# Kernel optimization log

Hardware: AMD Instinct MI355X
Metric: run time of the kernel (lower is better)

Reference implementation:

```python
import jax, jax.numpy as jnp
from jax import lax
import numpy as np

B, N, E, U = 128, 1024, 300, 128
L = 512          # num_leaves per sample
NN = 2 * L - 1   # num_nodes per sample (binary tree)


def _hsig(x):
    # Keras hard_sigmoid: clip(0.2*x + 0.5, 0, 1)
    return jnp.clip(0.2 * x + 0.5, 0.0, 1.0)


def setup_inputs() -> dict:
    key = jax.random.key(0)
    ks = jax.random.split(key, 5)
    rng = np.random.default_rng(0)
    # children of node t are uniform in [0, t) -> valid bottom-up binary tree
    u = rng.random((B, N, 2))
    child = (u * np.arange(N)[None, :, None]).astype(np.int32)
    child[:, :L, :] = 0  # leaves have no children (never read)
    num_vecs = np.tile(np.array([[NN, L]], np.int32), (B, 1))
    return {
        "initial_state": jax.random.normal(ks[0], (B, N, E), jnp.float32),
        "translation_kernel": jax.random.normal(ks[1], (E, U), jnp.float32) * 0.05,
        "kernel": jax.random.normal(ks[2], (5 * U, U), jnp.float32) * 0.05,
        "recurrent_kernel": jax.random.normal(ks[3], (5 * U, 2 * U), jnp.float32) * 0.05,
        "bias": jnp.zeros((5 * U, 1), jnp.float32),
        "child_vecs": jnp.asarray(child),
        "num_vecs": jnp.asarray(num_vecs),
    }


def reference(initial_state, translation_kernel, kernel, recurrent_kernel, bias,
              child_vecs, num_vecs):
    b, n, _ = initial_state.shape
    units = kernel.shape[1]
    # leaf initial states: relu(x @ W_translate)  -> [B, N, U]
    x = jax.nn.relu(jnp.einsum('bne,eu->bnu', initial_state, translation_kernel))
    num_nodes = num_vecs[:, 0]
    num_leaves = num_vecs[:, 1]
    bvec = bias[:, 0][None, :]  # [1, 5U]

    def step(carry, t):
        H, C = carry  # [B, N, U] each
        ch = jnp.take(child_vecs, t, axis=1)                                   # [B, 2]
        h_ch = jnp.take_along_axis(H, ch[:, :, None], axis=1).reshape(b, 2 * units)
        c_ch = jnp.take_along_axis(C, ch[:, :, None], axis=1).reshape(b, 2 * units)
        xt = jnp.take(x, t, axis=1)                                            # [B, U]
        # z = kernel @ x^T + recurrent_kernel @ [h_l; h_r] + bias  (batched, [B, 5U])
        z = xt @ kernel.T + h_ch @ recurrent_kernel.T + bvec
        i = _hsig(z[:, :units])
        f = _hsig(z[:, units:3 * units])                                       # [B, 2U]
        o = _hsig(z[:, 3 * units:4 * units])
        g = jnp.tanh(z[:, 4 * units:])
        # faithful to original: reshape (flat_mem*f) as [U, 2] row-major, sum axis 1
        c_new = (c_ch * f).reshape(b, units, 2).sum(axis=-1) + i * g
        h_new = o * jnp.tanh(c_new)
        act = ((t >= num_leaves) & (t < num_nodes))[:, None]                   # [B, 1]
        h_upd = jnp.where(act, h_new, jnp.take(H, t, axis=1))
        c_upd = jnp.where(act, c_new, jnp.take(C, t, axis=1))
        H = lax.dynamic_update_slice(H, h_upd[:, None, :], (0, t, 0))
        C = lax.dynamic_update_slice(C, c_upd[:, None, :], (0, t, 0))
        return (H, C), None

    # leaves start with hidden = memory = translated vec; internal nodes overwritten in order
    (H, _), _ = lax.scan(step, (x, x), jnp.arange(n))
    valid = (jnp.arange(n)[None, :] < num_nodes[:, None])[..., None]
    return H * valid.astype(H.dtype)
```

## Files before the change

### kernel.cpp

```cpp
#include <hip/hip_runtime.h>
#include <hip/hip_bf16.h>

#define B_ 128
#define N_ 1024
#define E_ 300
#define U_ 128
#define M_ (B_ * N_)
#define Z_ (5 * U_)
#define LMAXT 40
#define LPAR 20

typedef __attribute__((ext_vector_type(8))) short bf16x8;
typedef __attribute__((ext_vector_type(4))) float f32x4;
typedef _Float16 f16x4 __attribute__((ext_vector_type(4)));
typedef _Float16 f16x8 __attribute__((ext_vector_type(8)));

__device__ __forceinline__ short f2bf(float f) {
  unsigned u = __builtin_bit_cast(unsigned, f);
  u = (u + 0x7fffu + ((u >> 16) & 1u)) >> 16;
  return (short)u;
}

__device__ __forceinline__ float hsig(float z) {
  float v = __builtin_fmaf(z, 0.2f, 0.5f);
  v = v < 0.f ? 0.f : v;
  v = v > 1.f ? 1.f : v;
  return v;
}

__device__ __forceinline__ float tanh_fast(float x) {
  float p = __expf(2.f * x);
  return 1.f - 2.f * __builtin_amdgcn_rcpf(p + 1.f);
}

__device__ __forceinline__ unsigned pk2(float a, float b) {
  return __builtin_bit_cast(unsigned, __builtin_amdgcn_cvt_pkrtz(a, b));
}

__device__ __forceinline__ f16x8 pack8(float4 a, float4 b) {
  uint4 u;
  u.x = pk2(a.x, a.y);
  u.y = pk2(a.z, a.w);
  u.z = pk2(b.x, b.y);
  u.w = pk2(b.z, b.w);
  return __builtin_bit_cast(f16x8, u);
}

__global__ __launch_bounds__(256) void prep(
    const float* __restrict__ Wr, const float* __restrict__ Wk,
    _Float16* __restrict__ W16, _Float16* __restrict__ Wk16) {
  const int idx = blockIdx.x * 256 + threadIdx.x;
  if (idx < 163840) {
    W16[idx] = (_Float16)Wr[idx];
  } else if (idx < 245760) {
    const int i = idx - 163840;
    Wk16[i] = (_Float16)Wk[i];
  }
}

__global__ __launch_bounds__(256) void x_gemm(
    const float* __restrict__ A, const float* __restrict__ W,
    float* __restrict__ H) {
  __shared__ __align__(16) short As[64][40];
  __shared__ __align__(16) short Ws[128][40];
  const int tid = threadIdx.x;
  const int m0 = blockIdx.x * 64;
  f32x4 acc[8] = {};
  const int lane = tid & 63, wv = tid >> 6;
  const int lr = lane & 15, lg = lane >> 4;

  for (int kc = 0; kc < 10; ++kc) {
    const int k0 = kc * 32;
    {
      const int row = tid >> 2, kk = (tid & 3) * 8;
      const float* src = A + (size_t)(m0 + row) * E_ + k0 + kk;
      bf16x8 v;
      if (k0 + 32 <= E_) {
#pragma unroll
        for (int i = 0; i < 8; ++i) v[i] = f2bf(src[i]);
      } else {
#pragma unroll
        for (int i = 0; i < 8; ++i)
          v[i] = (k0 + kk + i < E_) ? f2bf(src[i]) : (short)0;
      }
      *(bf16x8*)&As[row][kk] = v;
    }
#pragma unroll
    for (int s = 0; s < 2; ++s) {
      const int slot = tid + s * 256;
      const int n = slot & 127, kg = slot >> 7;
      bf16x8 v;
      if (k0 + 32 <= E_) {
#pragma unroll
        for (int i = 0; i < 8; ++i) v[i] = f2bf(W[(k0 + kg * 8 + i) * U_ + n]);
      } else {
#pragma unroll
        for (int i = 0; i < 8; ++i) {
          const int k = k0 + kg * 8 + i;
          v[i] = (k < E_) ? f2bf(W[k * U_ + n]) : (short)0;
        }
      }
      *(bf16x8*)&Ws[n][kg * 8] = v;
    }
    __syncthreads();
    bf16x8 a = *(const bf16x8*)&As[wv * 16 + lr][lg * 8];
#pragma unroll
    for (int nt = 0; nt < 8; ++nt) {
      bf16x8 b = *(const bf16x8*)&Ws[nt * 16 + lr][lg * 8];
      acc[nt] = __builtin_amdgcn_mfma_f32_16x16x32_bf16(a, b, acc[nt], 0, 0, 0);
    }
    __syncthreads();
  }
#pragma unroll
  for (int nt = 0; nt < 8; ++nt) {
#pragma unroll
    for (int r = 0; r < 4; ++r) {
      const int m = m0 + wv * 16 + lg * 4 + r;
      const int n = nt * 16 + lr;
      float v = acc[nt][r];
      v = v > 0.f ? v : 0.f;
      H[(size_t)m * U_ + n] = v;
    }
  }
}

__global__ __launch_bounds__(256) void xz_gemm(
    const float* __restrict__ X, const _Float16* __restrict__ Wk16,
    const float* __restrict__ bias, const int* __restrict__ nv,
    _Float16* __restrict__ XZ) {
  const int m0 = blockIdx.x * 64;
  {
    const int bb = m0 >> 10;
    const int t0 = m0 & (N_ - 1);
    const int nodes = nv[2 * bb], leaves = nv[2 * bb + 1];
    if (t0 + 64 <= leaves || t0 >= nodes) return;
  }
  __shared__ __align__(16) short As[64][40];
  __shared__ __align__(16) short Ws[128][40];
  __shared__ __align__(16) _Float16 xzls[64][136];
  const int tid = threadIdx.x;
  const int n0 = blockIdx.y * 128;
  f32x4 acc[8] = {};
  const int lane = tid & 63, wv = tid >> 6;
  const int lr = lane & 15, lg = lane >> 4;

  for (int kc = 0; kc < 4; ++kc) {
    const int k0 = kc * 32;
    {
      const int row = tid >> 2, kk = (tid & 3) * 8;
      const float* src = X + (size_t)(m0 + row) * U_ + k0 + kk;
      const float4 a0 = *(const float4*)src;
      const float4 a1 = *(const float4*)(src + 4);
      *(f16x8*)&As[row][kk] = pack8(a0, a1);
    }
#pragma unroll
    for (int s = 0; s < 2; ++s) {
      const int slot = tid + s * 256;
      const int n = slot >> 2, kk = (slot & 3) * 8;
      *(f16x8*)&Ws[n][kk] =
          *(const f16x8*)(Wk16 + (size_t)(n0 + n) * U_ + k0 + kk);
    }
    __syncthreads();
    f16x8 a = *(const f16x8*)&As[wv * 16 + lr][lg * 8];
#pragma unroll
    for (int nt = 0; nt < 8; ++nt) {
      f16x8 b = *(const f16x8*)&Ws[nt * 16 + lr][lg * 8];
      acc[nt] = __builtin_amdgcn_mfma_f32_16x16x32_f16(a, b, acc[nt], 0, 0, 0);
    }
    __syncthreads();
  }
#pragma unroll
  for (int nt = 0; nt < 8; ++nt) {
    const float bv = bias[n0 + nt * 16 + lr];
#pragma unroll
    for (int r = 0; r < 4; ++r)
      xzls[wv * 16 + lg * 4 + r][nt * 16 + lr] = (_Float16)(acc[nt][r] + bv);
  }
  __syncthreads();
  {
    const int row = tid >> 2, c0 = (tid & 3) * 32;
    _Float16* dst = XZ + (size_t)(m0 + row) * Z_ + n0 + c0;
#pragma unroll
    for (int s = 0; s < 4; ++s)
      *(f16x8*)(dst + 8 * s) = *(const f16x8*)&xzls[row][c0 + 8 * s];
  }
}

__global__ __launch_bounds__(512) void levelize(
    const int* __restrict__ child, const int* __restrict__ nv,
    unsigned char* __restrict__ lv, short* __restrict__ rank,
    int* __restrict__ cnt) {
  const int b = blockIdx.x;
  const int tid = threadIdx.x;
  int nodes = nv[2 * b];
  int leaves = nv[2 * b + 1];
  if (nodes > N_) nodes = N_;
  if (leaves < 0) leaves = 0;

  __shared__ short lvs[N_];
  __shared__ int chs[2 * N_];
  __shared__ int cnts[LMAXT];
  __shared__ int changed;

  for (int i = tid; i < N_; i += 512) lvs[i] = 0;
  for (int i = tid; i < 2 * N_; i += 512) chs[i] = child[(size_t)b * 2 * N_ + i];
  if (tid < LMAXT) cnts[tid] = 0;
  __syncthreads();

  int stable = 0;
  for (int s = 0; s < 64; ++s) {
    if (tid == 0) changed = 0;
    __syncthreads();
    int any = 0;
    for (int t = leaves + tid; t < nodes; t += 512) {
      const int c0 = chs[2 * t], c1 = chs[2 * t + 1];
      const int l0 = (c0 < t && c0 >= 0) ? lvs[c0] : 0;
      const int l1 = (c1 < t && c1 >= 0) ? lvs[c1] : 0;
      const int l = 1 + (l0 > l1 ? l0 : l1);
      if (l > (int)lvs[t]) { lvs[t] = (short)l; any = 1; }
    }
    if (any) changed = 1;
    __syncthreads();
    if (!changed) { stable = 1; break; }
  }
  if (!stable) {
    if (tid == 0) {
      for (int t = leaves; t < nodes; ++t) {
        const int c0 = chs[2 * t], c1 = chs[2 * t + 1];
        const int l0 = (c0 < t && c0 >= 0) ? lvs[c0] : 0;
        const int l1 = (c1 < t && c1 >= 0) ? lvs[c1] : 0;
        lvs[t] = (short)(1 + (l0 > l1 ? l0 : l1));
      }
    }
    __syncthreads();
  }

  for (int t = tid; t < nodes; t += 512) {
    int l = (t < leaves) ? 0 : (int)lvs[t];
    if (l > LMAXT - 1) l = LMAXT - 1;
    lv[b * N_ + t] = (unsigned char)l;
    if (t >= leaves && l < LMAXT - 1)
      rank[b * N_ + t] = (short)atomicAdd(&cnts[l], 1);
  }
  __syncthreads();
  if (tid == 0) {
    for (int t = leaves; t < nodes; ++t)
      if ((int)lvs[t] >= LMAXT - 1) rank[b * N_ + t] = (short)(cnts[LMAXT - 1]++);
  }
  __syncthreads();
  if (tid < LMAXT) cnt[tid * 128 + b] = cnts[tid];
}

__global__ __launch_bounds__(64) void offsets(
    const int* __restrict__ cnt, int* __restrict__ pos, int* __restrict__ goff) {
  const int l = threadIdx.x;
  __shared__ int tot[LMAXT];
  if (l < LMAXT) {
    int s = 0;
    for (int b = 0; b < 128; ++b) {
      pos[l * 128 + b] = s;
      s += cnt[l * 128 + b];
    }
    tot[l] = s;
  }
  __syncthreads();
  if (l == 0) {
    int g = 0;
    for (int i = 0; i < LMAXT; ++i) { goff[i] = g; g += tot[i]; }
    goff[LMAXT] = g;
  }
  __syncthreads();
  if (l < LMAXT) {
    const int g = goff[l];
    for (int b = 0; b < 128; ++b) pos[l * 128 + b] += g;
  }
}

__global__ __launch_bounds__(256) void scatter_zero(
    const int* __restrict__ nv, const unsigned char* __restrict__ lv,
    const short* __restrict__ rank, const int* __restrict__ pos,
    int* __restrict__ glist, float* __restrict__ H) {
  const int b = blockIdx.x;
  const int tid = threadIdx.x;
  int nodes = nv[2 * b];
  int leaves = nv[2 * b + 1];
  if (nodes > N_) nodes = N_;
  if (leaves < 0) leaves = 0;
  for (int t = leaves + tid; t < nodes; t += 256) {
    const int l = lv[b * N_ + t];
    glist[pos[l * 128 + b] + rank[b * N_ + t]] = (b << 10) | t;
  }
  const int total = (N_ - nodes) * U_;
  for (int idx = tid; idx < total; idx += 256)
    H[(size_t)b * N_ * U_ + nodes * U_ + idx] = 0.f;
}

struct ChunkLd {
  float4 a0, a1;
  float4 cv0, cv1;
  f16x4 xzi, xzo, xzg;
  f16x8 xzf;
  int nid, rem;
};

__device__ __forceinline__ ChunkLd load_chunk(
    int chunk, int nchunk, int base, int count, const int* __restrict__ glist,
    const int* __restrict__ child, const unsigned char* __restrict__ lv,
    const _Float16* __restrict__ XZ, const float* __restrict__ H,
    const float* __restrict__ C, int j, int s, int col, int u0, int mc) {
  ChunkLd r;
  const int cc = chunk < nchunk - 1 ? chunk : nchunk - 1;
  const int cb = base + cc * 16;
  int rem = count - cc * 16;
  if (rem > 16) rem = 16;
  r.rem = rem;

  const int nidj = glist[cb + (j < rem ? j : rem - 1)];
  const int bj = nidj >> 10, tj = nidj & 1023;
  const int chj = child[((size_t)bj << 11) + 2 * tj + (s >> 4)];
  const float* hsrc = H + (((size_t)(bj << 10) + chj) << 7) + ((s & 15) << 3);
  r.a0 = *(const float4*)hsrc;
  r.a1 = *(const float4*)(hsrc + 4);

  const int nidc = glist[cb + (col < rem ? col : rem - 1)];
  r.nid = nidc;
  const _Float16* xzr = XZ + (size_t)nidc * Z_;
  r.xzi = *(const f16x4*)(xzr + u0);
  r.xzf = *(const f16x8*)(xzr + 128 + mc);
  r.xzo = *(const f16x4*)(xzr + 384 + u0);
  r.xzg = *(const f16x4*)(xzr + 512 + u0);
  const int bc = nidc >> 10, tc = nidc & 1023;
  const int csel = child[((size_t)bc << 11) + 2 * tc + (mc >> 7)];
  const int crow = (bc << 10) | csel;
  const float* cbp =
      (lv[crow] == 0 ? H : C) + ((size_t)crow << 7) + (mc & 127);
  r.cv0 = ((const float4*)cbp)[0];
  r.cv1 = ((const float4*)cbp)[1];
  return r;
}

__global__ __launch_bounds__(512, 2) void level_gemm(
    int lvl, const _Float16* __restrict__ W16, const int* __restrict__ child,
    const unsigned char* __restrict__ lv, const int* __restrict__ goff,
    const int* __restrict__ glist, const _Float16* __restrict__ XZ,
    float* __restrict__ H, float* __restrict__ C) {
  const int base = goff[lvl];
  const int count = goff[lvl + 1] - base;
  if (count <= 0) return;
  const int nchunk = (count + 15) >> 4;
  if ((int)blockIdx.x >= nchunk) return;
  const int tid = threadIdx.x;
  const int lane = tid & 63, w = tid >> 6;
  const int col = lane & 15, hi = lane >> 4;
  const int u0 = 16 * w + 4 * hi;
  const int mc = 2 * u0;
  const int j = tid >> 5, s = tid & 31;

  f16x8 afrag[5][8];
  {
    const int rows[5] = {16 * w + col, 128 + 32 * w + 2 * col,
                         129 + 32 * w + 2 * col, 384 + 16 * w + col,
                         512 + 16 * w + col};
#pragma unroll
    for (int rt = 0; rt < 5; ++rt) {
      const _Float16* rs = W16 + (size_t)rows[rt] * 256 + 8 * hi;
#pragma unroll
      for (int kt = 0; kt < 8; ++kt) afrag[rt][kt] = *(const f16x8*)(rs + 32 * kt);
    }
  }

  __shared__ __align__(16) _Float16 hbuf[2][16][272];

  ChunkLd cur = load_chunk(blockIdx.x, nchunk, base, count, glist, child, lv,
                           XZ, H, C, j, s, col, u0, mc);
  int p = 0;
  for (int chunk = blockIdx.x; chunk < nchunk; chunk += gridDim.x) {
    uint4 hp;
    hp.x = pk2(cur.a0.x, cur.a0.y);
    hp.y = pk2(cur.a0.z, cur.a0.w);
    hp.z = pk2(cur.a1.x, cur.a1.y);
    hp.w = pk2(cur.a1.z, cur.a1.w);
    *(uint4*)&hbuf[p][j][(s >> 4) * 128 + (s & 15) * 8] = hp;

    ChunkLd nxt = load_chunk(chunk + gridDim.x < nchunk ? chunk + gridDim.x
                                                        : nchunk - 1,
                             nchunk, base, count, glist, child, lv, XZ, H, C,
                             j, s, col, u0, mc);

    asm volatile("s_waitcnt lgkmcnt(0)" ::: "memory");
    __builtin_amdgcn_sched_barrier(0);
    __builtin_amdgcn_s_barrier();
    __builtin_amdgcn_sched_barrier(0);

    f32x4 acc[5];
#pragma unroll
    for (int r = 0; r < 4; ++r) {
      acc[0][r] = (float)cur.xzi[r];
      acc[1][r] = (float)cur.xzf[2 * r];
      acc[2][r] = (float)cur.xzf[2 * r + 1];
      acc[3][r] = (float)cur.xzo[r];
      acc[4][r] = (float)cur.xzg[r];
    }
#pragma unroll
    for (int kt = 0; kt < 8; ++kt) {
      const f16x8 bf = *(const f16x8*)&hbuf[p][col][32 * kt + 8 * hi];
#pragma unroll
      for (int rt = 0; rt < 5; ++rt)
        acc[rt] = __builtin_amdgcn_mfma_f32_16x16x32_f16(afrag[rt][kt], bf,
                                                         acc[rt], 0, 0, 0);
    }

    const float ce[8] = {cur.cv0.x, cur.cv0.y, cur.cv0.z, cur.cv0.w,
                         cur.cv1.x, cur.cv1.y, cur.cv1.z, cur.cv1.w};
    f32x4 hn4, cn4;
#pragma unroll
    for (int r = 0; r < 4; ++r) {
      const float cn = ce[2 * r] * hsig(acc[1][r]) +
                       ce[2 * r + 1] * hsig(acc[2][r]) +
                       hsig(acc[0][r]) * tanh_fast(acc[4][r]);
      cn4[r] = cn;
      hn4[r] = hsig(acc[3][r]) * tanh_fast(cn);
    }
    if (col < cur.rem) {
      const size_t rowb = (size_t)cur.nid << 7;
      *(f32x4*)(H + rowb + u0) = hn4;
      *(f32x4*)(C + rowb + u0) = cn4;
    }
    cur = nxt;
    p ^= 1;
  }
}

__global__ __launch_bounds__(512, 2) void tail_scan(
    const _Float16* __restrict__ W16, const int* __restrict__ child,
    const unsigned char* __restrict__ lv, const int* __restrict__ nv,
    const int* __restrict__ pos, const int* __restrict__ cnt,
    const int* __restrict__ glist, const _Float16* __restrict__ XZ,
    float* __restrict__ H, float* __restrict__ C) {
  const int b = blockIdx.x;
  const int tid = threadIdx.x;
  const int lane = tid & 63, w = tid >> 6;
  const int col = lane & 15, hi = lane >> 4;
  const int u0 = 16 * w + 4 * hi;
  const int mc = 2 * u0;
  const int m4 = 4 * lane;

  f16x8 afrag[5][8];
  {
    const int rows[5] = {16 * w + col, 128 + 32 * w + 2 * col,
                         129 + 32 * w + 2 * col, 384 + 16 * w + col,
                         512 + 16 * w + col};
#pragma unroll
    for (int rt = 0; rt < 5; ++rt) {
      const _Float16* rs = W16 + (size_t)rows[rt] * 256 + 8 * hi;
#pragma unroll
      for (int kt = 0; kt < 8; ++kt) afrag[rt][kt] = *(const f16x8*)(rs + 32 * kt);
    }
  }

  __shared__ __align__(16) _Float16 hb1[256];
  const int* chb = child + (size_t)b * 2 * N_;
  const unsigned char* lvb = lv + (size_t)b * N_;
  float* Hb = H + (size_t)b * N_ * U_;
  float* Cb = C + (size_t)b * N_ * U_;
  const _Float16* xzb = XZ + (size_t)b * N_ * Z_;

  for (int l = LPAR; l < LMAXT; ++l) {
    const int p0 = pos[l * 128 + b];
    const int n = cnt[l * 128 + b];
    for (int i = 0; i < n; ++i) {
      const int t = glist[p0 + i] & 1023;
      if (tid < 64) {
        const int ch = chb[2 * t + (m4 >> 7)];
        const float4 hv = *(const float4*)(Hb + ((size_t)ch << 7) + (m4 & 127));
        uint2 hp;
        hp.x = pk2(hv.x, hv.y);
        hp.y = pk2(hv.z, hv.w);
        *(uint2*)&hb1[m4] = hp;
      }
      const int cs = chb[2 * t + (mc >> 7)];
      const float* cbp =
          (lvb[cs] == 0 ? Hb : Cb) + ((size_t)cs << 7) + (mc & 127);
      const float4 cv0 = ((const float4*)cbp)[0];
      const float4 cv1 = ((const float4*)cbp)[1];
      const _Float16* xzr = xzb + (size_t)t * Z_;
      const f16x4 xzi = *(const f16x4*)(xzr + u0);
      const f16x8 xzf = *(const f16x8*)(xzr + 128 + mc);
      const f16x4 xzo = *(const f16x4*)(xzr + 384 + u0);
      const f16x4 xzg = *(const f16x4*)(xzr + 512 + u0);
      __syncthreads();
      f32x4 acc[5];
#pragma unroll
      for (int r = 0; r < 4; ++r) {
        acc[0][r] = (float)xzi[r];
        acc[1][r] = (float)xzf[2 * r];
        acc[2][r] = (float)xzf[2 * r + 1];
        acc[3][r] = (float)xzo[r];
        acc[4][r] = (float)xzg[r];
      }
#pragma unroll
      for (int kt = 0; kt < 8; ++kt) {
        const f16x8 bf = *(const f16x8*)&hb1[32 * kt + 8 * hi];
#pragma unroll
        for (int rt = 0; rt < 5; ++rt)
          acc[rt] = __builtin_amdgcn_mfma_f32_16x16x32_f16(afrag[rt][kt], bf,
                                                           acc[rt], 0, 0, 0);
      }
      const float ce[8] = {cv0.x, cv0.y, cv0.z, cv0.w,
                           cv1.x, cv1.y, cv1.z, cv1.w};
      f32x4 hn4, cn4;
#pragma unroll
      for (int r = 0; r < 4; ++r) {
        const float cn = ce[2 * r] * hsig(acc[1][r]) +
                         ce[2 * r + 1] * hsig(acc[2][r]) +
                         hsig(acc[0][r]) * tanh_fast(acc[4][r]);
        cn4[r] = cn;
        hn4[r] = hsig(acc[3][r]) * tanh_fast(cn);
      }
      if (col == 0) {
        *(f32x4*)(Hb + ((size_t)t << 7) + u0) = hn4;
        *(f32x4*)(Cb + ((size_t)t << 7) + u0) = cn4;
      }
      __syncthreads();
    }
  }
}

extern "C" void kernel_launch(void* const* d_in, const int* in_sizes, int n_in,
                              void* d_out, int out_size, void* d_ws,
                              size_t ws_size, hipStream_t stream) {
  const float* state = (const float*)d_in[0];
  const float* tk    = (const float*)d_in[1];
  const float* Wk    = (const float*)d_in[2];
  const float* Wr    = (const float*)d_in[3];
  const float* bias  = (const float*)d_in[4];
  const int*   child = (const int*)d_in[5];
  const int*   nvp   = (const int*)d_in[6];
  float* H = (float*)d_out;

  char* wsb = (char*)d_ws;
  _Float16* W16   = (_Float16*)(wsb + 0x000000);
  _Float16* Wk16  = (_Float16*)(wsb + 0x050000);
  unsigned char* lv = (unsigned char*)(wsb + 0x078000);
  short* rank     = (short*)(wsb + 0x098000);
  int* cnt        = (int*)(wsb + 0x0D8000);
  int* pos        = (int*)(wsb + 0x0DD000);
  int* goff       = (int*)(wsb + 0x0E2000);
  int* glist      = (int*)(wsb + 0x0E3000);
  const size_t meta_sz = 2ull * 1024 * 1024;
  const size_t c_bytes = (size_t)M_ * U_ * sizeof(float);
  float* C = (float*)(wsb + meta_sz);
  _Float16* XZ = (_Float16*)(wsb + meta_sz + c_bytes);

  prep<<<960, 256, 0, stream>>>(Wr, Wk, W16, Wk16);
  x_gemm<<<M_ / 64, 256, 0, stream>>>(state, tk, H);
  xz_gemm<<<dim3(M_ / 64, 5), 256, 0, stream>>>(H, Wk16, bias, nvp, XZ);
  levelize<<<B_, 512, 0, stream>>>(child, nvp, lv, rank, cnt);
  offsets<<<1, 64, 0, stream>>>(cnt, pos, goff);
  scatter_zero<<<B_, 256, 0, stream>>>(nvp, lv, rank, pos, glist, H);
  static const int lg[LPAR] = {0,  512, 384, 256, 192, 128, 96, 64, 48, 32,
                               24, 20,  16,  16,  16,  16,  16, 16, 16, 16};
  for (int l = 1; l < LPAR; ++l)
    level_gemm<<<lg[l], 512, 0, stream>>>(l, W16, child, lv, goff, glist, XZ,
                                          H, C);
  tail_scan<<<B_, 512, 0, stream>>>(W16, child, lv, nvp, pos, cnt, glist, XZ,
                                    H, C);
}
```

Before: 427.4 us.

## Pre-transpose translation kernel, seed C from x_gemm, retune level split

```diff
diff --git a/kernel.cpp b/kernel.cpp
--- a/kernel.cpp
+++ b/kernel.cpp
@@ -8,7 +8,7 @@
 #define M_ (B_ * N_)
 #define Z_ (5 * U_)
 #define LMAXT 40
-#define LPAR 20
+#define LPAR 14
 
 typedef __attribute__((ext_vector_type(8))) short bf16x8;
 typedef __attribute__((ext_vector_type(4))) float f32x4;
@@ -48,23 +48,30 @@
 
 __global__ __launch_bounds__(256) void prep(
     const float* __restrict__ Wr, const float* __restrict__ Wk,
-    _Float16* __restrict__ W16, _Float16* __restrict__ Wk16) {
+    const float* __restrict__ tk, _Float16* __restrict__ W16,
+    _Float16* __restrict__ Wk16, short* __restrict__ tkTb) {
   const int idx = blockIdx.x * 256 + threadIdx.x;
   if (idx < 163840) {
     W16[idx] = (_Float16)Wr[idx];
   } else if (idx < 245760) {
     const int i = idx - 163840;
     Wk16[i] = (_Float16)Wk[i];
+  } else if (idx < 286720) {
+    const int i = idx - 245760;
+    const int n = i / 320, k = i - n * 320;
+    tkTb[i] = (k < E_) ? f2bf(tk[k * U_ + n]) : (short)0;
   }
 }
 
 __global__ __launch_bounds__(256) void x_gemm(
-    const float* __restrict__ A, const float* __restrict__ W,
-    float* __restrict__ H) {
+    const float* __restrict__ A, const short* __restrict__ tkTb,
+    const int* __restrict__ nv, float* __restrict__ H, float* __restrict__ C) {
   __shared__ __align__(16) short As[64][40];
   __shared__ __align__(16) short Ws[128][40];
   const int tid = threadIdx.x;
   const int m0 = blockIdx.x * 64;
+  const int nodes = nv[2 * (m0 >> 10)];
+  const int t0 = m0 & (N_ - 1);
   f32x4 acc[8] = {};
   const int lane = tid & 63, wv = tid >> 6;
   const int lr = lane & 15, lg = lane >> 4;
@@ -89,18 +96,8 @@
     for (int s = 0; s < 2; ++s) {
       const int slot = tid + s * 256;
       const int n = slot & 127, kg = slot >> 7;
-      bf16x8 v;
-      if (k0 + 32 <= E_) {
-#pragma unroll
-        for (int i = 0; i < 8; ++i) v[i] = f2bf(W[(k0 + kg * 8 + i) * U_ + n]);
-      } else {
-#pragma unroll
-        for (int i = 0; i < 8; ++i) {
-          const int k = k0 + kg * 8 + i;
-          v[i] = (k < E_) ? f2bf(W[k * U_ + n]) : (short)0;
-        }
-      }
-      *(bf16x8*)&Ws[n][kg * 8] = v;
+      *(bf16x8*)&Ws[n][kg * 8] =
+          *(const bf16x8*)(tkTb + (size_t)n * 320 + k0 + kg * 8);
     }
     __syncthreads();
     bf16x8 a = *(const bf16x8*)&As[wv * 16 + lr][lg * 8];
@@ -116,10 +113,13 @@
 #pragma unroll
     for (int r = 0; r < 4; ++r) {
       const int m = m0 + wv * 16 + lg * 4 + r;
+      const int trow = t0 + wv * 16 + lg * 4 + r;
       const int n = nt * 16 + lr;
       float v = acc[nt][r];
       v = v > 0.f ? v : 0.f;
+      if (trow >= nodes) v = 0.f;
       H[(size_t)m * U_ + n] = v;
+      C[(size_t)m * U_ + n] = v;
     }
   }
 }
@@ -235,12 +235,11 @@
     __syncthreads();
   }
 
-  for (int t = tid; t < nodes; t += 512) {
-    int l = (t < leaves) ? 0 : (int)lvs[t];
+  for (int t = leaves + tid; t < nodes; t += 512) {
+    int l = lvs[t];
     if (l > LMAXT - 1) l = LMAXT - 1;
     lv[b * N_ + t] = (unsigned char)l;
-    if (t >= leaves && l < LMAXT - 1)
-      rank[b * N_ + t] = (short)atomicAdd(&cnts[l], 1);
+    if (l < LMAXT - 1) rank[b * N_ + t] = (short)atomicAdd(&cnts[l], 1);
   }
   __syncthreads();
   if (tid == 0) {
@@ -276,10 +275,10 @@
   }
 }
 
-__global__ __launch_bounds__(256) void scatter_zero(
+__global__ __launch_bounds__(256) void scatter(
     const int* __restrict__ nv, const unsigned char* __restrict__ lv,
     const short* __restrict__ rank, const int* __restrict__ pos,
-    int* __restrict__ glist, float* __restrict__ H) {
+    int* __restrict__ glist) {
   const int b = blockIdx.x;
   const int tid = threadIdx.x;
   int nodes = nv[2 * b];
@@ -290,9 +289,6 @@
     const int l = lv[b * N_ + t];
     glist[pos[l * 128 + b] + rank[b * N_ + t]] = (b << 10) | t;
   }
-  const int total = (N_ - nodes) * U_;
-  for (int idx = tid; idx < total; idx += 256)
-    H[(size_t)b * N_ * U_ + nodes * U_ + idx] = 0.f;
 }
 
 struct ChunkLd {
@@ -305,9 +301,9 @@
 
 __device__ __forceinline__ ChunkLd load_chunk(
     int chunk, int nchunk, int base, int count, const int* __restrict__ glist,
-    const int* __restrict__ child, const unsigned char* __restrict__ lv,
-    const _Float16* __restrict__ XZ, const float* __restrict__ H,
-    const float* __restrict__ C, int j, int s, int col, int u0, int mc) {
+    const int* __restrict__ child, const _Float16* __restrict__ XZ,
+    const float* __restrict__ H, const float* __restrict__ C, int j, int s,
+    int col, int u0, int mc) {
   ChunkLd r;
   const int cc = chunk < nchunk - 1 ? chunk : nchunk - 1;
   const int cb = base + cc * 16;
@@ -331,9 +327,7 @@
   r.xzg = *(const f16x4*)(xzr + 512 + u0);
   const int bc = nidc >> 10, tc = nidc & 1023;
   const int csel = child[((size_t)bc << 11) + 2 * tc + (mc >> 7)];
-  const int crow = (bc << 10) | csel;
-  const float* cbp =
-      (lv[crow] == 0 ? H : C) + ((size_t)crow << 7) + (mc & 127);
+  const float* cbp = C + (((size_t)(bc << 10) + csel) << 7) + (mc & 127);
   r.cv0 = ((const float4*)cbp)[0];
   r.cv1 = ((const float4*)cbp)[1];
   return r;
@@ -341,9 +335,9 @@
 
 __global__ __launch_bounds__(512, 2) void level_gemm(
     int lvl, const _Float16* __restrict__ W16, const int* __restrict__ child,
-    const unsigned char* __restrict__ lv, const int* __restrict__ goff,
-    const int* __restrict__ glist, const _Float16* __restrict__ XZ,
-    float* __restrict__ H, float* __restrict__ C) {
+    const int* __restrict__ goff, const int* __restrict__ glist,
+    const _Float16* __restrict__ XZ, float* __restrict__ H,
+    float* __restrict__ C) {
   const int base = goff[lvl];
   const int count = goff[lvl + 1] - base;
   if (count <= 0) return;
@@ -371,8 +365,8 @@
 
   __shared__ __align__(16) _Float16 hbuf[2][16][272];
 
-  ChunkLd cur = load_chunk(blockIdx.x, nchunk, base, count, glist, child, lv,
-                           XZ, H, C, j, s, col, u0, mc);
+  ChunkLd cur = load_chunk(blockIdx.x, nchunk, base, count, glist, child, XZ,
+                           H, C, j, s, col, u0, mc);
   int p = 0;
   for (int chunk = blockIdx.x; chunk < nchunk; chunk += gridDim.x) {
     uint4 hp;
@@ -384,8 +378,8 @@
 
     ChunkLd nxt = load_chunk(chunk + gridDim.x < nchunk ? chunk + gridDim.x
                                                         : nchunk - 1,
-                             nchunk, base, count, glist, child, lv, XZ, H, C,
-                             j, s, col, u0, mc);
+                             nchunk, base, count, glist, child, XZ, H, C, j, s,
+                             col, u0, mc);
 
     asm volatile("s_waitcnt lgkmcnt(0)" ::: "memory");
     __builtin_amdgcn_sched_barrier(0);
@@ -433,10 +427,10 @@
 
 __global__ __launch_bounds__(512, 2) void tail_scan(
     const _Float16* __restrict__ W16, const int* __restrict__ child,
-    const unsigned char* __restrict__ lv, const int* __restrict__ nv,
-    const int* __restrict__ pos, const int* __restrict__ cnt,
-    const int* __restrict__ glist, const _Float16* __restrict__ XZ,
-    float* __restrict__ H, float* __restrict__ C) {
+    const int* __restrict__ nv, const int* __restrict__ pos,
+    const int* __restrict__ cnt, const int* __restrict__ glist,
+    const _Float16* __restrict__ XZ, float* __restrict__ H,
+    float* __restrict__ C) {
   const int b = blockIdx.x;
   const int tid = threadIdx.x;
   const int lane = tid & 63, w = tid >> 6;
@@ -460,7 +454,6 @@
 
   __shared__ __align__(16) _Float16 hb1[256];
   const int* chb = child + (size_t)b * 2 * N_;
-  const unsigned char* lvb = lv + (size_t)b * N_;
   float* Hb = H + (size_t)b * N_ * U_;
   float* Cb = C + (size_t)b * N_ * U_;
   const _Float16* xzb = XZ + (size_t)b * N_ * Z_;
@@ -479,8 +472,7 @@
         *(uint2*)&hb1[m4] = hp;
       }
       const int cs = chb[2 * t + (mc >> 7)];
-      const float* cbp =
-          (lvb[cs] == 0 ? Hb : Cb) + ((size_t)cs << 7) + (mc & 127);
+      const float* cbp = Cb + ((size_t)cs << 7) + (mc & 127);
       const float4 cv0 = ((const float4*)cbp)[0];
       const float4 cv1 = ((const float4*)cbp)[1];
       const _Float16* xzr = xzb + (size_t)t * Z_;
@@ -541,28 +533,29 @@
   char* wsb = (char*)d_ws;
   _Float16* W16   = (_Float16*)(wsb + 0x000000);
   _Float16* Wk16  = (_Float16*)(wsb + 0x050000);
-  unsigned char* lv = (unsigned char*)(wsb + 0x078000);
-  short* rank     = (short*)(wsb + 0x098000);
-  int* cnt        = (int*)(wsb + 0x0D8000);
-  int* pos        = (int*)(wsb + 0x0DD000);
-  int* goff       = (int*)(wsb + 0x0E2000);
-  int* glist      = (int*)(wsb + 0x0E3000);
+  short* tkTb     = (short*)(wsb + 0x078000);
+  unsigned char* lv = (unsigned char*)(wsb + 0x08C000);
+  short* rank     = (short*)(wsb + 0x0AC000);
+  int* cnt        = (int*)(wsb + 0x0EC000);
+  int* pos        = (int*)(wsb + 0x0F1000);
+  int* goff       = (int*)(wsb + 0x0F6000);
+  int* glist      = (int*)(wsb + 0x0F7000);
   const size_t meta_sz = 2ull * 1024 * 1024;
   const size_t c_bytes = (size_t)M_ * U_ * sizeof(float);
   float* C = (float*)(wsb + meta_sz);
   _Float16* XZ = (_Float16*)(wsb + meta_sz + c_bytes);
 
-  prep<<<960, 256, 0, stream>>>(Wr, Wk, W16, Wk16);
-  x_gemm<<<M_ / 64, 256, 0, stream>>>(state, tk, H);
+  prep<<<1120, 256, 0, stream>>>(Wr, Wk, tk, W16, Wk16, tkTb);
+  x_gemm<<<M_ / 64, 256, 0, stream>>>(state, tkTb, nvp, H, C);
   xz_gemm<<<dim3(M_ / 64, 5), 256, 0, stream>>>(H, Wk16, bias, nvp, XZ);
   levelize<<<B_, 512, 0, stream>>>(child, nvp, lv, rank, cnt);
   offsets<<<1, 64, 0, stream>>>(cnt, pos, goff);
-  scatter_zero<<<B_, 256, 0, stream>>>(nvp, lv, rank, pos, glist, H);
-  static const int lg[LPAR] = {0,  512, 384, 256, 192, 128, 96, 64, 48, 32,
-                               24, 20,  16,  16,  16,  16,  16, 16, 16, 16};
+  scatter<<<B_, 256, 0, stream>>>(nvp, lv, rank, pos, glist);
+  static const int lg[LPAR] = {0, 512, 512, 256, 256, 128, 128,
+                               64, 64, 64, 32, 32, 32, 32};
   for (int l = 1; l < LPAR; ++l)
-    level_gemm<<<lg[l], 512, 0, stream>>>(l, W16, child, lv, goff, glist, XZ,
-                                          H, C);
-  tail_scan<<<B_, 512, 0, stream>>>(W16, child, lv, nvp, pos, cnt, glist, XZ,
-                                    H, C);
-}
+    level_gemm<<<lg[l], 512, 0, stream>>>(l, W16, child, goff, glist, XZ, H,
+                                          C);
+  tail_scan<<<B_, 512, 0, stream>>>(W16, child, nvp, pos, cnt, glist, XZ, H,
+                                    C);
+}
```

After: 426.6 us. No clear change (-0.2%).
